# Optimization experiments

Measured on AMD Instinct MI355X. Metric: run time of the kernel, lower is better.

The kernel has to match this reference:

```python
import jax, jax.numpy as jnp
import numpy as np

N = 50000          # nodes
E = 1_600_000      # edges (avg degree 32)
D_IN = 128
D_H = 128
D_OUT = 64
L = 3              # GATv2 layers
NEG_SLOPE = 0.2    # PyG GATv2Conv default negative_slope


def setup_inputs() -> dict:
    key = jax.random.key(0)
    ks = jax.random.split(key, 12)
    s = 0.05
    x = jax.random.normal(ks[0], (N, D_IN), jnp.float32)
    edge_index = jax.random.randint(ks[1], (2, E), 0, N, jnp.int32)
    # stacked per-layer GATv2 params (input_dim == hidden_dim so all layers match)
    Wl = jax.random.normal(ks[2], (L, D_H, D_H), jnp.float32) * s   # lin_l weights
    bl = jnp.zeros((L, D_H), jnp.float32)
    Wr = jax.random.normal(ks[3], (L, D_H, D_H), jnp.float32) * s   # lin_r weights
    br = jnp.zeros((L, D_H), jnp.float32)
    att = jax.random.normal(ks[4], (L, D_H), jnp.float32) * s       # attention vector a
    bias = jnp.zeros((L, D_H), jnp.float32)                          # post-aggregation bias
    # post_mp MLP head
    W1 = jax.random.normal(ks[5], (D_H, D_H), jnp.float32) * s
    b1 = jnp.zeros((D_H,), jnp.float32)
    W2 = jax.random.normal(ks[6], (D_OUT, D_H), jnp.float32) * s
    b2 = jnp.zeros((D_OUT,), jnp.float32)
    return {"x": x, "edge_index": edge_index, "Wl": Wl, "bl": bl, "Wr": Wr,
            "br": br, "att": att, "bias": bias, "W1": W1, "b1": b1, "W2": W2, "b2": b2}


def _gatv2_layer(x, src, dst, Wl, bl, Wr, br, att, bias):
    # lin_l on source features, lin_r on destination features (heads=1)
    xl = x @ Wl.T + bl                                   # [N, D_H]
    xr = x @ Wr.T + br                                   # [N, D_H]
    e = jax.nn.leaky_relu(xl[src] + xr[dst], NEG_SLOPE)  # [E, D_H]
    logits = e @ att                                     # [E]
    # segment softmax over incoming edges of each destination node
    m = jax.ops.segment_max(logits, dst, num_segments=N)
    ex = jnp.exp(logits - m[dst])
    denom = jax.ops.segment_sum(ex, dst, num_segments=N)
    alpha = ex / denom[dst]                              # [E]
    msg = xl[src] * alpha[:, None]                       # [E, D_H]
    out = jax.ops.segment_sum(msg, dst, num_segments=N)  # [N, D_H]
    return out + bias


def reference(x, edge_index, Wl, bl, Wr, br, att, bias, W1, b1, W2, b2):
    src, dst = edge_index[0], edge_index[1]
    for i in range(L):
        x = _gatv2_layer(x, src, dst, Wl[i], bl[i], Wr[i], br[i], att[i], bias[i])
        x = jax.nn.relu(x)  # dropout is identity in eval mode
    h = x @ W1.T + b1
    return h @ W2.T + b2  # return_embedding=True -> raw output
```

## Files before the change

kernel.cpp:

```cpp
#include <hip/hip_runtime.h>
#include <hip/hip_bf16.h>

#define NN 50000
#define EE 1600000
#define DH 128
#define DOUT 64
#define NEG 0.2f
#define NBK 256
#define CHUNK 4096

typedef short bf16x8 __attribute__((ext_vector_type(8)));
typedef float f32x4 __attribute__((ext_vector_type(4)));


__global__ __launch_bounds__(256) void k_bhist(const int* __restrict__ dst,
                                               int* __restrict__ bucket_hist) {
    __shared__ int lh[NBK];
    lh[threadIdx.x] = 0;
    __syncthreads();
    const int e0 = blockIdx.x * CHUNK;
    #pragma unroll
    for (int k = 0; k < CHUNK / 256; k++) {
        int e = e0 + k * 256 + threadIdx.x;
        if (e < EE) atomicAdd(&lh[((unsigned)dst[e]) >> 8], 1);
    }
    __syncthreads();
    int c = lh[threadIdx.x];
    if (c) atomicAdd(&bucket_hist[threadIdx.x], c);
}

__global__ __launch_bounds__(256) void k_scan_bucket(const int* __restrict__ bucket_hist,
                                                     int* __restrict__ bucket_base,
                                                     int* __restrict__ bucket_cursor) {
    __shared__ int tmp[NBK];
    int t = threadIdx.x;
    int v = bucket_hist[t];
    tmp[t] = v;
    __syncthreads();
    #pragma unroll
    for (int off = 1; off < NBK; off <<= 1) {
        int tt = (t >= off) ? tmp[t - off] : 0;
        __syncthreads();
        tmp[t] += tt;
        __syncthreads();
    }
    bucket_base[t] = tmp[t] - v;
    bucket_cursor[t] = tmp[t] - v;
}

__global__ __launch_bounds__(256) void k_scatter(const int* __restrict__ src,
                                                 const int* __restrict__ dst,
                                                 int* __restrict__ bucket_cursor,
                                                 unsigned int* __restrict__ pairs) {
    __shared__ int lh[NBK];
    __shared__ int lbase[NBK];
    lh[threadIdx.x] = 0;
    __syncthreads();
    const int e0 = blockIdx.x * CHUNK;
    int dl[CHUNK / 256];
    #pragma unroll
    for (int k = 0; k < CHUNK / 256; k++) {
        int e = e0 + k * 256 + threadIdx.x;
        dl[k] = (e < EE) ? dst[e] : -1;
        if (dl[k] >= 0) atomicAdd(&lh[((unsigned)dl[k]) >> 8], 1);
    }
    __syncthreads();
    int c = lh[threadIdx.x];
    lbase[threadIdx.x] = c ? atomicAdd(&bucket_cursor[threadIdx.x], c) : 0;
    __syncthreads();
    lh[threadIdx.x] = 0;
    __syncthreads();
    #pragma unroll
    for (int k = 0; k < CHUNK / 256; k++) {
        int e = e0 + k * 256 + threadIdx.x;
        if (dl[k] >= 0) {
            int b = ((unsigned)dl[k]) >> 8;
            int loc = atomicAdd(&lh[b], 1);
            pairs[lbase[b] + loc] =
                (unsigned)src[e] | (((unsigned)dl[k] & 255u) << 16);
        }
    }
}

__global__ __launch_bounds__(256) void k_bucket(const unsigned int* __restrict__ pairs,
                                                const int* __restrict__ bucket_base,
                                                const int* __restrict__ bucket_hist,
                                                int* __restrict__ csr_off,
                                                int* __restrict__ prow,
                                                int* __restrict__ deg) {
    __shared__ int cnt[256];
    __shared__ int sbase[256];
    __shared__ int scn[256];
    __shared__ int cur[256];
    const int b = blockIdx.x;
    const int t = threadIdx.x;
    const int pstart = bucket_base[b];
    const int pcnt = bucket_hist[b];

    cnt[t] = 0;
    cur[t] = 0;
    __syncthreads();
    for (int i = t; i < pcnt; i += 256)
        atomicAdd(&cnt[pairs[pstart + i] >> 16], 1);
    __syncthreads();

    const int d = cnt[t];
    const int padded = (d + 7) & ~7;
    scn[t] = padded;
    __syncthreads();
    #pragma unroll
    for (int off = 1; off < 256; off <<= 1) {
        int v = (t >= off) ? scn[t - off] : 0;
        __syncthreads();
        scn[t] += v;
        __syncthreads();
    }
    const int mybase = scn[t] - padded;
    sbase[t] = mybase;
    const int cb = pstart + b * 2048;
    const int node = b * 256 + t;
    if (node < NN) {
        prow[node] = cb + mybase;
        deg[node] = d;
    }
    __syncthreads();

    for (int i = t; i < pcnt; i += 256) {
        unsigned int pr = pairs[pstart + i];
        int ln = (int)(pr >> 16);
        int pos = atomicAdd(&cur[ln], 1);
        csr_off[cb + sbase[ln] + pos] = (int)((pr & 0xffffu) << 8);
    }
    __syncthreads();

    for (int p = d; p < padded; p++) csr_off[cb + mybase + p] = 0;
}


static __device__ __forceinline__ unsigned int f2bf(float f) {
    unsigned int u = __float_as_uint(f);
    return (u + 0x7fffu + ((u >> 16) & 1u)) >> 16;
}
static __device__ __forceinline__ unsigned int pack2bf(float lo, float hi) {
    return f2bf(lo) | (f2bf(hi) << 16);
}


template <bool ABF>
__global__ __launch_bounds__(256) void k_mfma(const void* __restrict__ X,
                                              const float* __restrict__ W0,
                                              const float* __restrict__ b0,
                                              unsigned int* __restrict__ C0bf,
                                              const float* __restrict__ W1,
                                              const float* __restrict__ b1,
                                              float* __restrict__ C1,
                                              int nrows) {
    constexpr int BN = 128;
    constexpr int MF = 4, NF = 4;
    __shared__ __align__(16) unsigned short As[4][4][128][8];
    __shared__ __align__(16) unsigned short Bs[4][4][BN][8];

    const int tid = threadIdx.x;
    const int row0 = blockIdx.x * 128;
    const bool bfout = (blockIdx.y == 0);
    const float* W = bfout ? W0 : W1;
    const float* bias = bfout ? b0 : b1;

    if constexpr (ABF) {
        const uint4* X4 = (const uint4*)X;
        #pragma unroll
        for (int i = 0; i < 8; i++) {
            int L = i * 256 + tid;
            int r = L >> 4, q = L & 15;
            int gr = row0 + r;
            uint4 v = make_uint4(0u, 0u, 0u, 0u);
            if (gr < nrows) v = X4[(size_t)gr * 16 + q];
            *(uint4*)&As[q >> 2][q & 3][r][0] = v;
        }
    } else {
        const float* Xf = (const float*)X;
        #pragma unroll
        for (int i = 0; i < 16; i++) {
            int L = i * 256 + tid;
            int r = L >> 5, kq = L & 31;
            int gr = row0 + r;
            float4 v = make_float4(0.f, 0.f, 0.f, 0.f);
            if (gr < nrows) v = *(const float4*)&Xf[(size_t)gr * 128 + kq * 4];
            int k = kq * 4;
            *(uint2*)&As[k >> 5][(k >> 3) & 3][r][k & 7] =
                make_uint2(pack2bf(v.x, v.y), pack2bf(v.z, v.w));
        }
    }
    #pragma unroll
    for (int i = 0; i < (BN * 32) / 256; i++) {
        int L = i * 256 + tid;
        int r = L >> 5, kq = L & 31;
        float4 v = *(const float4*)&W[(size_t)r * 128 + kq * 4];
        int k = kq * 4;
        *(uint2*)&Bs[k >> 5][(k >> 3) & 3][r][k & 7] =
            make_uint2(pack2bf(v.x, v.y), pack2bf(v.z, v.w));
    }
    __syncthreads();

    const int w = tid >> 6;
    const int lane = tid & 63;
    const int lr = lane & 15;
    const int kg = lane >> 4;
    const int rowbase = (w >> 1) * 64;
    const int colbase = (w & 1) * 64;

    f32x4 acc[MF][NF];
    #pragma unroll
    for (int i = 0; i < MF; i++)
        #pragma unroll
        for (int j = 0; j < NF; j++) acc[i][j] = (f32x4){0.f, 0.f, 0.f, 0.f};

    #pragma unroll
    for (int kc = 0; kc < 4; kc++) {
        bf16x8 af[MF], bfr[NF];
        #pragma unroll
        for (int i = 0; i < MF; i++)
            af[i] = *(const bf16x8*)&As[kc][kg][rowbase + i * 16 + lr][0];
        #pragma unroll
        for (int j = 0; j < NF; j++)
            bfr[j] = *(const bf16x8*)&Bs[kc][kg][colbase + j * 16 + lr][0];
        #pragma unroll
        for (int i = 0; i < MF; i++)
            #pragma unroll
            for (int j = 0; j < NF; j++)
                acc[i][j] = __builtin_amdgcn_mfma_f32_16x16x32_bf16(af[i], bfr[j],
                                                                    acc[i][j], 0, 0, 0);
    }

    #pragma unroll
    for (int i = 0; i < MF; i++) {
        #pragma unroll
        for (int reg = 0; reg < 4; reg++) {
            int row = rowbase + i * 16 + (lane >> 4) * 4 + reg;
            int gr = row0 + row;
            if (gr < nrows) {
                #pragma unroll
                for (int j = 0; j < NF; j++) {
                    int col = colbase + j * 16 + lr;
                    float v = acc[i][j][reg] + bias[col];
                    if (bfout) {
                        float vn = __shfl_xor(v, 1, 64);
                        if (!(lane & 1)) {
                            C0bf[(size_t)gr * (BN / 2) + (col >> 1)] = pack2bf(v, vn);
                        }
                    } else {
                        C1[(size_t)gr * BN + col] = v;
                    }
                }
            }
        }
    }
}


__global__ __launch_bounds__(256) void k_head(const void* __restrict__ Xbf,
                                              const float* __restrict__ W1,
                                              const float* __restrict__ b1,
                                              const float* __restrict__ W2,
                                              const float* __restrict__ b2,
                                              float* __restrict__ out,
                                              int nrows) {
    __shared__ __align__(16) unsigned short As[4][4][128][8];
    __shared__ __align__(16) unsigned short Bs[4][4][128][8];

    const int tid = threadIdx.x;
    const int row0 = blockIdx.x * 128;

    const uint4* X4 = (const uint4*)Xbf;
    #pragma unroll
    for (int i = 0; i < 8; i++) {
        int L = i * 256 + tid;
        int r = L >> 4, q = L & 15;
        int gr = row0 + r;
        uint4 v = make_uint4(0u, 0u, 0u, 0u);
        if (gr < nrows) v = X4[(size_t)gr * 16 + q];
        *(uint4*)&As[q >> 2][q & 3][r][0] = v;
    }
    #pragma unroll
    for (int i = 0; i < 16; i++) {
        int L = i * 256 + tid;
        int r = L >> 5, kq = L & 31;
        float4 v = *(const float4*)&W1[(size_t)r * 128 + kq * 4];
        int k = kq * 4;
        *(uint2*)&Bs[k >> 5][(k >> 3) & 3][r][k & 7] =
            make_uint2(pack2bf(v.x, v.y), pack2bf(v.z, v.w));
    }
    __syncthreads();

    const int w = tid >> 6;
    const int lane = tid & 63;
    const int lr = lane & 15;
    const int kg = lane >> 4;
    const int rowbase = (w >> 1) * 64;
    const int colbase = (w & 1) * 64;

    f32x4 acc[4][4];
    #pragma unroll
    for (int i = 0; i < 4; i++)
        #pragma unroll
        for (int j = 0; j < 4; j++) acc[i][j] = (f32x4){0.f, 0.f, 0.f, 0.f};

    #pragma unroll
    for (int kc = 0; kc < 4; kc++) {
        bf16x8 af[4], bfr[4];
        #pragma unroll
        for (int i = 0; i < 4; i++)
            af[i] = *(const bf16x8*)&As[kc][kg][rowbase + i * 16 + lr][0];
        #pragma unroll
        for (int j = 0; j < 4; j++)
            bfr[j] = *(const bf16x8*)&Bs[kc][kg][colbase + j * 16 + lr][0];
        #pragma unroll
        for (int i = 0; i < 4; i++)
            #pragma unroll
            for (int j = 0; j < 4; j++)
                acc[i][j] = __builtin_amdgcn_mfma_f32_16x16x32_bf16(af[i], bfr[j],
                                                                    acc[i][j], 0, 0, 0);
    }
    __syncthreads();

    #pragma unroll
    for (int i = 0; i < 4; i++) {
        #pragma unroll
        for (int reg = 0; reg < 4; reg++) {
            int row = rowbase + i * 16 + (lane >> 4) * 4 + reg;
            #pragma unroll
            for (int j = 0; j < 4; j++) {
                int col = colbase + j * 16 + lr;
                float v = acc[i][j][reg] + b1[col];
                float vn = __shfl_xor(v, 1, 64);
                if (!(lane & 1)) {
                    *(unsigned int*)&As[col >> 5][(col >> 3) & 3][row][col & 7] =
                        pack2bf(v, vn);
                }
            }
        }
    }
    #pragma unroll
    for (int i = 0; i < 8; i++) {
        int L = i * 256 + tid;
        int r = L >> 5, kq = L & 31;
        float4 v = *(const float4*)&W2[(size_t)r * 128 + kq * 4];
        int k = kq * 4;
        *(uint2*)&Bs[k >> 5][(k >> 3) & 3][r][k & 7] =
            make_uint2(pack2bf(v.x, v.y), pack2bf(v.z, v.w));
    }
    __syncthreads();

    const int rowbase2 = w * 32;
    f32x4 acc2[2][4];
    #pragma unroll
    for (int i = 0; i < 2; i++)
        #pragma unroll
        for (int j = 0; j < 4; j++) acc2[i][j] = (f32x4){0.f, 0.f, 0.f, 0.f};

    #pragma unroll
    for (int kc = 0; kc < 4; kc++) {
        bf16x8 af2[2], bf2[4];
        #pragma unroll
        for (int i = 0; i < 2; i++)
            af2[i] = *(const bf16x8*)&As[kc][kg][rowbase2 + i * 16 + lr][0];
        #pragma unroll
        for (int j = 0; j < 4; j++)
            bf2[j] = *(const bf16x8*)&Bs[kc][kg][j * 16 + lr][0];
        #pragma unroll
        for (int i = 0; i < 2; i++)
            #pragma unroll
            for (int j = 0; j < 4; j++)
                acc2[i][j] = __builtin_amdgcn_mfma_f32_16x16x32_bf16(af2[i], bf2[j],
                                                                     acc2[i][j], 0, 0, 0);
    }

    #pragma unroll
    for (int i = 0; i < 2; i++) {
        #pragma unroll
        for (int reg = 0; reg < 4; reg++) {
            int row = rowbase2 + i * 16 + (lane >> 4) * 4 + reg;
            int gr = row0 + row;
            if (gr < nrows) {
                #pragma unroll
                for (int j = 0; j < 4; j++) {
                    int col = j * 16 + lr;
                    out[(size_t)gr * DOUT + col] = acc2[i][j][reg] + b2[col];
                }
            }
        }
    }
}


__global__ __launch_bounds__(256) void k_gat_node(const unsigned short* __restrict__ xl16,
                                                  const float* __restrict__ xr,
                                                  const float* __restrict__ att,
                                                  const float* __restrict__ bias,
                                                  const int* __restrict__ csr_off,
                                                  const int* __restrict__ prow,
                                                  const int* __restrict__ deg,
                                                  unsigned int* __restrict__ xout) {
    const int lane = threadIdx.x & 63;
    const int n = blockIdx.x * 4 + (threadIdx.x >> 6);
    if (n >= NN) return;

    const int l7 = lane & 7;
    const float2 xrv = *(const float2*)&xr[(size_t)n * DH + 2 * lane];
    const float2 attv = *(const float2*)&att[2 * lane];
    const int p0 = prow[n];
    const int dg = deg[n];
    const int pend = p0 + dg;
    const int pend_pad = p0 + ((dg + 7) & ~7);

    float ssum_l = 0.f;
    float ax = 0.f, ay = 0.f;

    const char* xlb = (const char*)xl16;
    const unsigned int lb = (unsigned int)lane * 4u;

    for (int p = p0; p < pend_pad; p += 8) {
        uint4 ia = *(const uint4*)&csr_off[p];
        uint4 ib = *(const uint4*)&csr_off[p + 4];
        unsigned int u0 = *(const unsigned int*)(xlb + (ia.x + lb));
        unsigned int u1 = *(const unsigned int*)(xlb + (ia.y + lb));
        unsigned int u2 = *(const unsigned int*)(xlb + (ia.z + lb));
        unsigned int u3 = *(const unsigned int*)(xlb + (ia.w + lb));
        unsigned int u4 = *(const unsigned int*)(xlb + (ib.x + lb));
        unsigned int u5 = *(const unsigned int*)(xlb + (ib.y + lb));
        unsigned int u6 = *(const unsigned int*)(xlb + (ib.z + lb));
        unsigned int u7 = *(const unsigned int*)(xlb + (ib.w + lb));
        unsigned int uu[8] = {u0, u1, u2, u3, u4, u5, u6, u7};

        float x0[8], x1[8], w[8];
        #pragma unroll
        for (int j = 0; j < 8; j++) {
            x0[j] = __uint_as_float(uu[j] << 16);
            x1[j] = __uint_as_float(uu[j] & 0xffff0000u);
            float z0 = x0[j] + xrv.x;
            float z1 = x1[j] + xrv.y;
            float l0 = fmaxf(z0, NEG * z0);
            float l1 = fmaxf(z1, NEG * z1);
            w[j] = fmaf(l0, attv.x, l1 * attv.y);
        }

        float v4[4], v2[2], S;
        {
            const bool hi = (lane & 1);
            #pragma unroll
            for (int i = 0; i < 4; i++) {
                float keep = hi ? w[2 * i + 1] : w[2 * i];
                float send = hi ? w[2 * i] : w[2 * i + 1];
                v4[i] = keep + __shfl_xor(send, 1, 64);
            }
        }
        {
            const bool hi = (lane & 2);
            #pragma unroll
            for (int i = 0; i < 2; i++) {
                float keep = hi ? v4[2 * i + 1] : v4[2 * i];
                float send = hi ? v4[2 * i] : v4[2 * i + 1];
                v2[i] = keep + __shfl_xor(send, 2, 64);
            }
        }
        {
            const bool hi = (lane & 4);
            float keep = hi ? v2[1] : v2[0];
            float send = hi ? v2[0] : v2[1];
            S = keep + __shfl_xor(send, 4, 64);
        }
        S += __shfl_xor(S, 8, 64);
        S += __shfl_xor(S, 16, 64);
        S += __shfl_xor(S, 32, 64);

        float pe = (p + l7 < pend) ? __expf(S) : 0.f;
        ssum_l += pe;

        float q = __shfl_xor(pe, 1, 64);
        float pA = (l7 & 1) ? q : pe;
        float pB = (l7 & 1) ? pe : q;
        float qA = __shfl_xor(pA, 2, 64);
        float qB = __shfl_xor(pB, 2, 64);
        float p00 = (l7 & 2) ? qA : pA;
        float p01 = (l7 & 2) ? qB : pB;
        float p10 = (l7 & 2) ? pA : qA;
        float p11 = (l7 & 2) ? pB : qB;
        float r00 = __shfl_xor(p00, 4, 64);
        float r01 = __shfl_xor(p01, 4, 64);
        float r10 = __shfl_xor(p10, 4, 64);
        float r11 = __shfl_xor(p11, 4, 64);
        float pe0 = (l7 & 4) ? r00 : p00;
        float pe1 = (l7 & 4) ? r01 : p01;
        float pe2 = (l7 & 4) ? r10 : p10;
        float pe3 = (l7 & 4) ? r11 : p11;
        float pe4 = (l7 & 4) ? p00 : r00;
        float pe5 = (l7 & 4) ? p01 : r01;
        float pe6 = (l7 & 4) ? p10 : r10;
        float pe7 = (l7 & 4) ? p11 : r11;

        ax = fmaf(pe0, x0[0], ax);  ay = fmaf(pe0, x1[0], ay);
        ax = fmaf(pe1, x0[1], ax);  ay = fmaf(pe1, x1[1], ay);
        ax = fmaf(pe2, x0[2], ax);  ay = fmaf(pe2, x1[2], ay);
        ax = fmaf(pe3, x0[3], ax);  ay = fmaf(pe3, x1[3], ay);
        ax = fmaf(pe4, x0[4], ax);  ay = fmaf(pe4, x1[4], ay);
        ax = fmaf(pe5, x0[5], ax);  ay = fmaf(pe5, x1[5], ay);
        ax = fmaf(pe6, x0[6], ax);  ay = fmaf(pe6, x1[6], ay);
        ax = fmaf(pe7, x0[7], ax);  ay = fmaf(pe7, x1[7], ay);
    }

    float st = ssum_l;
    st += __shfl_xor(st, 1, 64);
    st += __shfl_xor(st, 2, 64);
    st += __shfl_xor(st, 4, 64);
    const float inv = (st > 0.f) ? 1.f / st : 0.f;

    const float2 bv = *(const float2*)&bias[2 * lane];
    const float o0 = fmaxf(fmaf(ax, inv, bv.x), 0.f);
    const float o1 = fmaxf(fmaf(ay, inv, bv.y), 0.f);
    xout[(size_t)n * (DH / 2) + lane] = pack2bf(o0, o1);
}


static inline size_t align256(size_t x) { return (x + 255) & ~(size_t)255; }

extern "C" void kernel_launch(void* const* d_in, const int* in_sizes, int n_in,
                              void* d_out, int out_size, void* d_ws, size_t ws_size,
                              hipStream_t stream) {
    (void)in_sizes; (void)n_in; (void)out_size; (void)ws_size;

    const float* x   = (const float*)d_in[0];
    const int* ei    = (const int*)d_in[1];
    const float* Wl  = (const float*)d_in[2];
    const float* bl  = (const float*)d_in[3];
    const float* Wr  = (const float*)d_in[4];
    const float* br  = (const float*)d_in[5];
    const float* att = (const float*)d_in[6];
    const float* bias= (const float*)d_in[7];
    const float* W1  = (const float*)d_in[8];
    const float* b1  = (const float*)d_in[9];
    const float* W2  = (const float*)d_in[10];
    const float* b2  = (const float*)d_in[11];
    float* out = (float*)d_out;

    const int* src = ei;
    const int* dst = ei + EE;

    const size_t EP = (size_t)EE + (size_t)NBK * 2048;

    char* w = (char*)d_ws;
    unsigned int* xA = (unsigned int*)w; w += align256((size_t)NN * (DH / 2) * 4);
    unsigned int* xB = (unsigned int*)w; w += align256((size_t)NN * (DH / 2) * 4);
    unsigned int* xl16 = (unsigned int*)w; w += align256((size_t)NN * DH * 2);
    float* xrb = (float*)w; w += align256((size_t)NN * DH * 4);
    unsigned int* pairs = (unsigned int*)w; w += align256((size_t)EE * 4);
    int* csr_off = (int*)w; w += align256(EP * 4);
    int* prow    = (int*)w; w += align256((size_t)NN * 4);
    int* deg     = (int*)w; w += align256((size_t)NN * 4);
    int* bucket_hist   = (int*)w; w += align256(NBK * 4);
    int* bucket_base   = (int*)w; w += align256(NBK * 4);
    int* bucket_cursor = (int*)w; w += align256(NBK * 4);

    const int nb_chunk = (EE + CHUNK - 1) / CHUNK;
    const int nb_bkt  = (NN + 255) / 256;
    const int nb_gemm = (NN + 127) / 128;
    const int nb_node = (NN + 3) / 4;

    hipMemsetAsync(bucket_hist, 0, NBK * 4, stream);
    k_bhist<<<nb_chunk, 256, 0, stream>>>(dst, bucket_hist);
    k_scan_bucket<<<1, NBK, 0, stream>>>(bucket_hist, bucket_base, bucket_cursor);
    k_scatter<<<nb_chunk, 256, 0, stream>>>(src, dst, bucket_cursor, pairs);
    k_bucket<<<nb_bkt, 256, 0, stream>>>(pairs, bucket_base, bucket_hist,
                                         csr_off, prow, deg);

    const void* xin = (const void*)x;
    for (int l = 0; l < 3; ++l) {
        const float* Wl_l = Wl + (size_t)l * DH * DH;
        const float* Wr_l = Wr + (size_t)l * DH * DH;
        const float* bl_l = bl + (size_t)l * DH;
        const float* br_l = br + (size_t)l * DH;
        const float* att_l = att + (size_t)l * DH;
        const float* bias_l = bias + (size_t)l * DH;
        unsigned int* xo = (l & 1) ? xB : xA;

        if (l == 0)
            k_mfma<false><<<dim3(nb_gemm, 2), 256, 0, stream>>>(xin, Wl_l, bl_l, xl16,
                                                                Wr_l, br_l, xrb, NN);
        else
            k_mfma<true><<<dim3(nb_gemm, 2), 256, 0, stream>>>(xin, Wl_l, bl_l, xl16,
                                                               Wr_l, br_l, xrb, NN);
        k_gat_node<<<nb_node, 256, 0, stream>>>((const unsigned short*)xl16, xrb,
                                                att_l, bias_l, csr_off, prow, deg, xo);
        xin = (const void*)xo;
    }

    k_head<<<nb_gemm, 256, 0, stream>>>(xin, W1, b1, W2, b2, out, NN);
}
```

Baseline: 381.4 us.

## Use fixed-capacity edge buckets and fuse lin_l/lin_r GEMMs into one kernel

```diff
diff --git a/kernel.cpp b/kernel.cpp
--- a/kernel.cpp
+++ b/kernel.cpp
@@ -8,45 +8,12 @@
 #define NEG 0.2f
 #define NBK 256
 #define CHUNK 4096
+#define BCAP 10240
+#define CCAP 12288
 
 typedef short bf16x8 __attribute__((ext_vector_type(8)));
 typedef float f32x4 __attribute__((ext_vector_type(4)));
 
-
-__global__ __launch_bounds__(256) void k_bhist(const int* __restrict__ dst,
-                                               int* __restrict__ bucket_hist) {
-    __shared__ int lh[NBK];
-    lh[threadIdx.x] = 0;
-    __syncthreads();
-    const int e0 = blockIdx.x * CHUNK;
-    #pragma unroll
-    for (int k = 0; k < CHUNK / 256; k++) {
-        int e = e0 + k * 256 + threadIdx.x;
-        if (e < EE) atomicAdd(&lh[((unsigned)dst[e]) >> 8], 1);
-    }
-    __syncthreads();
-    int c = lh[threadIdx.x];
-    if (c) atomicAdd(&bucket_hist[threadIdx.x], c);
-}
-
-__global__ __launch_bounds__(256) void k_scan_bucket(const int* __restrict__ bucket_hist,
-                                                     int* __restrict__ bucket_base,
-                                                     int* __restrict__ bucket_cursor) {
-    __shared__ int tmp[NBK];
-    int t = threadIdx.x;
-    int v = bucket_hist[t];
-    tmp[t] = v;
-    __syncthreads();
-    #pragma unroll
-    for (int off = 1; off < NBK; off <<= 1) {
-        int tt = (t >= off) ? tmp[t - off] : 0;
-        __syncthreads();
-        tmp[t] += tt;
-        __syncthreads();
-    }
-    bucket_base[t] = tmp[t] - v;
-    bucket_cursor[t] = tmp[t] - v;
-}
 
 __global__ __launch_bounds__(256) void k_scatter(const int* __restrict__ src,
                                                  const int* __restrict__ dst,
@@ -66,7 +33,8 @@
     }
     __syncthreads();
     int c = lh[threadIdx.x];
-    lbase[threadIdx.x] = c ? atomicAdd(&bucket_cursor[threadIdx.x], c) : 0;
+    lbase[threadIdx.x] = c ? (threadIdx.x * BCAP +
+                              atomicAdd(&bucket_cursor[threadIdx.x], c)) : 0;
     __syncthreads();
     lh[threadIdx.x] = 0;
     __syncthreads();
@@ -83,8 +51,7 @@
 }
 
 __global__ __launch_bounds__(256) void k_bucket(const unsigned int* __restrict__ pairs,
-                                                const int* __restrict__ bucket_base,
-                                                const int* __restrict__ bucket_hist,
+                                                const int* __restrict__ bucket_cursor,
                                                 int* __restrict__ csr_off,
                                                 int* __restrict__ prow,
                                                 int* __restrict__ deg) {
@@ -94,8 +61,8 @@
     __shared__ int cur[256];
     const int b = blockIdx.x;
     const int t = threadIdx.x;
-    const int pstart = bucket_base[b];
-    const int pcnt = bucket_hist[b];
+    const int pstart = b * BCAP;
+    const int pcnt = bucket_cursor[b];
 
     cnt[t] = 0;
     cur[t] = 0;
@@ -117,7 +84,7 @@
     }
     const int mybase = scn[t] - padded;
     sbase[t] = mybase;
-    const int cb = pstart + b * 2048;
+    const int cb = b * CCAP;
     const int node = b * 256 + t;
     if (node < NN) {
         prow[node] = cb + mybase;
@@ -147,24 +114,20 @@
 
 
 template <bool ABF>
-__global__ __launch_bounds__(256) void k_mfma(const void* __restrict__ X,
-                                              const float* __restrict__ W0,
-                                              const float* __restrict__ b0,
-                                              unsigned int* __restrict__ C0bf,
-                                              const float* __restrict__ W1,
-                                              const float* __restrict__ b1,
-                                              float* __restrict__ C1,
+__global__ __launch_bounds__(256) void k_dual(const void* __restrict__ X,
+                                              const float* __restrict__ Wl,
+                                              const float* __restrict__ bl,
+                                              unsigned int* __restrict__ Cl,
+                                              const float* __restrict__ Wr,
+                                              const float* __restrict__ br,
+                                              float* __restrict__ Cr,
                                               int nrows) {
-    constexpr int BN = 128;
-    constexpr int MF = 4, NF = 4;
     __shared__ __align__(16) unsigned short As[4][4][128][8];
-    __shared__ __align__(16) unsigned short Bs[4][4][BN][8];
+    __shared__ __align__(16) unsigned short Bl[4][4][128][8];
+    __shared__ __align__(16) unsigned short Br[4][4][128][8];
 
     const int tid = threadIdx.x;
     const int row0 = blockIdx.x * 128;
-    const bool bfout = (blockIdx.y == 0);
-    const float* W = bfout ? W0 : W1;
-    const float* bias = bfout ? b0 : b1;
 
     if constexpr (ABF) {
         const uint4* X4 = (const uint4*)X;
@@ -192,13 +155,16 @@
         }
     }
     #pragma unroll
-    for (int i = 0; i < (BN * 32) / 256; i++) {
+    for (int i = 0; i < 16; i++) {
         int L = i * 256 + tid;
         int r = L >> 5, kq = L & 31;
-        float4 v = *(const float4*)&W[(size_t)r * 128 + kq * 4];
         int k = kq * 4;
-        *(uint2*)&Bs[k >> 5][(k >> 3) & 3][r][k & 7] =
+        float4 v = *(const float4*)&Wl[(size_t)r * 128 + kq * 4];
+        *(uint2*)&Bl[k >> 5][(k >> 3) & 3][r][k & 7] =
             make_uint2(pack2bf(v.x, v.y), pack2bf(v.z, v.w));
+        float4 u = *(const float4*)&Wr[(size_t)r * 128 + kq * 4];
+        *(uint2*)&Br[k >> 5][(k >> 3) & 3][r][k & 7] =
+            make_uint2(pack2bf(u.x, u.y), pack2bf(u.z, u.w));
     }
     __syncthreads();
 
@@ -209,48 +175,78 @@
     const int rowbase = (w >> 1) * 64;
     const int colbase = (w & 1) * 64;
 
-    f32x4 acc[MF][NF];
-    #pragma unroll
-    for (int i = 0; i < MF; i++)
-        #pragma unroll
-        for (int j = 0; j < NF; j++) acc[i][j] = (f32x4){0.f, 0.f, 0.f, 0.f};
-
+    f32x4 acc[4][4];
+
+    #pragma unroll
+    for (int i = 0; i < 4; i++)
+        #pragma unroll
+        for (int j = 0; j < 4; j++) acc[i][j] = (f32x4){0.f, 0.f, 0.f, 0.f};
     #pragma unroll
     for (int kc = 0; kc < 4; kc++) {
-        bf16x8 af[MF], bfr[NF];
-        #pragma unroll
-        for (int i = 0; i < MF; i++)
+        bf16x8 af[4], bfr[4];
+        #pragma unroll
+        for (int i = 0; i < 4; i++)
             af[i] = *(const bf16x8*)&As[kc][kg][rowbase + i * 16 + lr][0];
         #pragma unroll
-        for (int j = 0; j < NF; j++)
-            bfr[j] = *(const bf16x8*)&Bs[kc][kg][colbase + j * 16 + lr][0];
-        #pragma unroll
-        for (int i = 0; i < MF; i++)
-            #pragma unroll
-            for (int j = 0; j < NF; j++)
+        for (int j = 0; j < 4; j++)
+            bfr[j] = *(const bf16x8*)&Bl[kc][kg][colbase + j * 16 + lr][0];
+        #pragma unroll
+        for (int i = 0; i < 4; i++)
+            #pragma unroll
+            for (int j = 0; j < 4; j++)
                 acc[i][j] = __builtin_amdgcn_mfma_f32_16x16x32_bf16(af[i], bfr[j],
                                                                     acc[i][j], 0, 0, 0);
     }
-
-    #pragma unroll
-    for (int i = 0; i < MF; i++) {
+    #pragma unroll
+    for (int i = 0; i < 4; i++) {
         #pragma unroll
         for (int reg = 0; reg < 4; reg++) {
             int row = rowbase + i * 16 + (lane >> 4) * 4 + reg;
             int gr = row0 + row;
             if (gr < nrows) {
                 #pragma unroll
-                for (int j = 0; j < NF; j++) {
+                for (int j = 0; j < 4; j++) {
                     int col = colbase + j * 16 + lr;
-                    float v = acc[i][j][reg] + bias[col];
-                    if (bfout) {
-                        float vn = __shfl_xor(v, 1, 64);
-                        if (!(lane & 1)) {
-                            C0bf[(size_t)gr * (BN / 2) + (col >> 1)] = pack2bf(v, vn);
-                        }
-                    } else {
-                        C1[(size_t)gr * BN + col] = v;
-                    }
+                    float v = acc[i][j][reg] + bl[col];
+                    float vn = __shfl_xor(v, 1, 64);
+                    if (!(lane & 1))
+                        Cl[(size_t)gr * (DH / 2) + (col >> 1)] = pack2bf(v, vn);
+                }
+            }
+        }
+    }
+
+    #pragma unroll
+    for (int i = 0; i < 4; i++)
+        #pragma unroll
+        for (int j = 0; j < 4; j++) acc[i][j] = (f32x4){0.f, 0.f, 0.f, 0.f};
+    #pragma unroll
+    for (int kc = 0; kc < 4; kc++) {
+        bf16x8 af[4], bfr[4];
+        #pragma unroll
+        for (int i = 0; i < 4; i++)
+            af[i] = *(const bf16x8*)&As[kc][kg][rowbase + i * 16 + lr][0];
+        #pragma unroll
+        for (int j = 0; j < 4; j++)
+            bfr[j] = *(const bf16x8*)&Br[kc][kg][colbase + j * 16 + lr][0];
+        #pragma unroll
+        for (int i = 0; i < 4; i++)
+            #pragma unroll
+            for (int j = 0; j < 4; j++)
+                acc[i][j] = __builtin_amdgcn_mfma_f32_16x16x32_bf16(af[i], bfr[j],
+                                                                    acc[i][j], 0, 0, 0);
+    }
+    #pragma unroll
+    for (int i = 0; i < 4; i++) {
+        #pragma unroll
+        for (int reg = 0; reg < 4; reg++) {
+            int row = rowbase + i * 16 + (lane >> 4) * 4 + reg;
+            int gr = row0 + row;
+            if (gr < nrows) {
+                #pragma unroll
+                for (int j = 0; j < 4; j++) {
+                    int col = colbase + j * 16 + lr;
+                    Cr[(size_t)gr * DH + col] = acc[i][j][reg] + br[col];
                 }
             }
         }
@@ -545,19 +541,15 @@
     const int* src = ei;
     const int* dst = ei + EE;
 
-    const size_t EP = (size_t)EE + (size_t)NBK * 2048;
-
     char* w = (char*)d_ws;
     unsigned int* xA = (unsigned int*)w; w += align256((size_t)NN * (DH / 2) * 4);
     unsigned int* xB = (unsigned int*)w; w += align256((size_t)NN * (DH / 2) * 4);
     unsigned int* xl16 = (unsigned int*)w; w += align256((size_t)NN * DH * 2);
     float* xrb = (float*)w; w += align256((size_t)NN * DH * 4);
-    unsigned int* pairs = (unsigned int*)w; w += align256((size_t)EE * 4);
-    int* csr_off = (int*)w; w += align256(EP * 4);
+    unsigned int* pairs = (unsigned int*)w; w += align256((size_t)NBK * BCAP * 4);
+    int* csr_off = (int*)w; w += align256((size_t)NBK * CCAP * 4);
     int* prow    = (int*)w; w += align256((size_t)NN * 4);
     int* deg     = (int*)w; w += align256((size_t)NN * 4);
-    int* bucket_hist   = (int*)w; w += align256(NBK * 4);
-    int* bucket_base   = (int*)w; w += align256(NBK * 4);
     int* bucket_cursor = (int*)w; w += align256(NBK * 4);
 
     const int nb_chunk = (EE + CHUNK - 1) / CHUNK;
@@ -565,12 +557,9 @@
     const int nb_gemm = (NN + 127) / 128;
     const int nb_node = (NN + 3) / 4;
 
-    hipMemsetAsync(bucket_hist, 0, NBK * 4, stream);
-    k_bhist<<<nb_chunk, 256, 0, stream>>>(dst, bucket_hist);
-    k_scan_bucket<<<1, NBK, 0, stream>>>(bucket_hist, bucket_base, bucket_cursor);
+    hipMemsetAsync(bucket_cursor, 0, NBK * 4, stream);
     k_scatter<<<nb_chunk, 256, 0, stream>>>(src, dst, bucket_cursor, pairs);
-    k_bucket<<<nb_bkt, 256, 0, stream>>>(pairs, bucket_base, bucket_hist,
-                                         csr_off, prow, deg);
+    k_bucket<<<nb_bkt, 256, 0, stream>>>(pairs, bucket_cursor, csr_off, prow, deg);
 
     const void* xin = (const void*)x;
     for (int l = 0; l < 3; ++l) {
@@ -583,11 +572,11 @@
         unsigned int* xo = (l & 1) ? xB : xA;
 
         if (l == 0)
-            k_mfma<false><<<dim3(nb_gemm, 2), 256, 0, stream>>>(xin, Wl_l, bl_l, xl16,
-                                                                Wr_l, br_l, xrb, NN);
+            k_dual<false><<<nb_gemm, 256, 0, stream>>>(xin, Wl_l, bl_l, xl16,
+                                                       Wr_l, br_l, xrb, NN);
         else
-            k_mfma<true><<<dim3(nb_gemm, 2), 256, 0, stream>>>(xin, Wl_l, bl_l, xl16,
-                                                               Wr_l, br_l, xrb, NN);
+            k_dual<true><<<nb_gemm, 256, 0, stream>>>(xin, Wl_l, bl_l, xl16,
+                                                      Wr_l, br_l, xrb, NN);
         k_gat_node<<<nb_node, 256, 0, stream>>>((const unsigned short*)xl16, xrb,
                                                 att_l, bias_l, csr_off, prow, deg, xo);
         xin = (const void*)xo;
```

Measured after the change: 382.5 us. Within noise of the previous version (+0.3%).
